# Kernel tuning notes

Hardware: AMD Instinct MI355X
Metric: run time of the kernel (lower is better)

The kernel has to match this reference:

```python
import jax, jax.numpy as jnp
import numpy as np

DEPTH = 10
LAMDA = 1e-3
EPS = 1e-7


def setup_inputs() -> dict:
    key = jax.random.key(0)
    k1, k2, k3, k4 = jax.random.split(key, 4)
    B, D, O = 16384, 512, 256
    N = 2 ** DEPTH - 1        # inner nodes
    L = 2 ** DEPTH            # leaves
    data = jax.random.normal(k1, (B, D), jnp.float32)
    # small scale on W keeps sigmoid away from saturation (like nn.Linear init)
    W = jax.random.normal(k2, (N, D + 1), jnp.float32) * 0.02
    beta = jax.random.normal(k3, (N,), jnp.float32)
    param = jax.random.normal(k4, (L, O), jnp.float32)
    return {"data": data, "W": W, "beta": beta, "param": param}


def reference(data, W, beta, param):
    B = data.shape[0]
    L = param.shape[0]
    # _data_augment_: prepend constant 1 as bias feature -> [B, D+1]
    x = jnp.concatenate([jnp.ones((B, 1), data.dtype), data], axis=1)
    # inner_nodes: sigmoid(beta * linear(x)) -> [B, N]
    p = jax.nn.sigmoid(beta * (x @ W.T))
    # per-node (go-left, go-right) probabilities -> [B, N, 2]
    path_prob = jnp.stack([p, 1.0 - p], axis=2)

    mu = jnp.ones((B, 1), data.dtype)          # path prob of root
    penalty = jnp.asarray(0.0, data.dtype)
    begin = 0
    for layer in range(DEPTH):                  # fixed small loop over depth
        n = 2 ** layer
        pp = path_prob[:, begin:begin + n, :].reshape(B, 2 * n)  # [B, 2n]
        mu_rep = jnp.repeat(mu, 2, axis=1)                        # [B, 2n]
        # vectorized form of the per-node penalty loop
        alpha = jnp.sum(pp * mu_rep, axis=0) / (jnp.sum(mu_rep, axis=0) + EPS)
        alpha = jnp.clip(alpha, EPS, 1.0 - EPS)
        coeff = LAMDA * (2.0 ** (-layer))
        penalty = penalty - coeff * 0.5 * jnp.sum(jnp.log(alpha) + jnp.log(1.0 - alpha))
        mu = mu_rep * pp
        begin += n

    # mu: [B, leaf_num]; leaf_nodes: mu @ softmax(param)
    dist = jax.nn.softmax(param, axis=1)       # [L, O]
    output = mu @ dist                          # [B, O]
    # greatest_path_probability: hard argmax leaf (one-hot @ dist == gather)
    ids = jnp.argmax(mu, axis=1)
    prediction = dist[ids]                      # [B, O]
    # LogProb=True
    return (jnp.log(prediction), jnp.log(output), penalty, W)
```

## Files before the change

### kernel.cpp

```cpp
#include <hip/hip_runtime.h>
#include <hip/hip_bf16.h>

#define B_ROWS 16384
#define DDIM   512
#define NNODES 1023
#define NLEAF  1024
#define ODIM   256
#define LAMDA  1e-3
#define EPSV   1e-7f

typedef __bf16 bf16x8v __attribute__((ext_vector_type(8)));
typedef _Float16 f16x8 __attribute__((ext_vector_type(8)));
typedef float  f32x16v __attribute__((ext_vector_type(16)));

__device__ __forceinline__ float bf2f(unsigned short u) {
    return __uint_as_float(((unsigned)u) << 16);
}

__device__ __forceinline__ void gload16h(const _Float16* g, _Float16* l) {
    __builtin_amdgcn_global_load_lds(
        (const __attribute__((address_space(1))) unsigned int*)g,
        (__attribute__((address_space(3))) unsigned int*)l, 16, 0, 0);
}
__device__ __forceinline__ void gload16b(const __hip_bfloat16* g, __hip_bfloat16* l) {
    __builtin_amdgcn_global_load_lds(
        (const __attribute__((address_space(1))) unsigned int*)g,
        (__attribute__((address_space(3))) unsigned int*)l, 16, 0, 0);
}

__global__ __launch_bounds__(256)
void prep_all(const float* __restrict__ data, const float* __restrict__ W,
              _Float16* __restrict__ Dh, _Float16* __restrict__ Dl,
              _Float16* __restrict__ Wh, _Float16* __restrict__ Wl,
              float* __restrict__ outW)
{
    if (blockIdx.x < 4096) {
        int idx = blockIdx.x * 256 + threadIdx.x;
        int b  = idx >> 6;
        int k8 = idx & 63;
        const float4 v0 = *reinterpret_cast<const float4*>(&data[(size_t)b * DDIM + k8 * 8]);
        const float4 v1 = *reinterpret_cast<const float4*>(&data[(size_t)b * DDIM + k8 * 8 + 4]);
        float a[8] = {v0.x, v0.y, v0.z, v0.w, v1.x, v1.y, v1.z, v1.w};
        __align__(16) _Float16 h[8], l[8];
#pragma unroll
        for (int j = 0; j < 8; ++j) {
            h[j] = (_Float16)a[j];
            l[j] = (_Float16)((a[j] - (float)h[j]) * 2048.f);
        }
        int by = b >> 8, tl = (b >> 5) & 7, ln = (b & 31) | ((k8 & 1) << 5), ks = k8 >> 1;
        size_t off = ((((size_t)by * 32 + ks) * 8 + tl) * 64 + ln) * 8;
        *reinterpret_cast<ulonglong2*>(&Dh[off]) = *reinterpret_cast<const ulonglong2*>(h);
        *reinterpret_cast<ulonglong2*>(&Dl[off]) = *reinterpret_cast<const ulonglong2*>(l);
    } else if (blockIdx.x < 4352) {
        int idx = (blockIdx.x - 4096) * 256 + threadIdx.x;
        int t  = idx & 255;
        int ks = (idx >> 8) & 31;
        int nb = idx >> 13;
        int tm = t >> 6, ln = t & 63;
        int node = nb * 128 + tm * 32 + (ln & 31);
        int k = ks * 16 + (ln >> 5) * 8;
        __align__(16) _Float16 h[8], l[8];
        if (node < NNODES) {
#pragma unroll
            for (int j = 0; j < 8; ++j) {
                float a = W[(size_t)node * 513 + 1 + k + j];
                h[j] = (_Float16)a;
                l[j] = (_Float16)((a - (float)h[j]) * 2048.f);
            }
        } else {
#pragma unroll
            for (int j = 0; j < 8; ++j) { h[j] = (_Float16)0.f; l[j] = (_Float16)0.f; }
        }
        size_t off = (size_t)idx * 8;
        *reinterpret_cast<ulonglong2*>(&Wh[off]) = *reinterpret_cast<const ulonglong2*>(h);
        *reinterpret_cast<ulonglong2*>(&Wl[off]) = *reinterpret_cast<const ulonglong2*>(l);
    } else {
        int i = (blockIdx.x - 4352) * 256 + threadIdx.x;
        if (i < NNODES * 513) outW[i] = W[i];
    }
}

__global__ __launch_bounds__(512, 2)
void gemm1_mfma(const _Float16* __restrict__ Wh, const _Float16* __restrict__ Wl,
                const _Float16* __restrict__ Dh, const _Float16* __restrict__ Dl,
                const float* __restrict__ W, const float* __restrict__ beta,
                float* __restrict__ PT)
{
    __shared__ _Float16 lds[2][24576];
    const int tid = threadIdx.x;
    const int lane = tid & 63;
    const int wv = tid >> 6;
    const int wm = wv & 1, wn = wv >> 1;
    const int id = blockIdx.x;
    const int xcd = id & 7, slot = id >> 3;
    const int bx = slot & 7;
    const int by = xcd * 8 + (slot >> 3);
    const size_t wofs = (size_t)bx * 65536 + tid * 8;
    const size_t dofs = (size_t)by * 131072 + tid * 8;

    f32x16v acc_h[2][2] = {};
    f32x16v acc_l[2][2] = {};

#define STAGE(buf, tt) do { \
        const size_t wo = wofs + (size_t)(tt) * 4096; \
        const size_t dd = dofs + (size_t)(tt) * 8192; \
        gload16h(Wh + wo,        &lds[buf][tid * 8]); \
        gload16h(Wl + wo,        &lds[buf][4096  + tid * 8]); \
        gload16h(Dh + dd,        &lds[buf][8192  + tid * 8]); \
        gload16h(Dh + dd + 4096, &lds[buf][12288 + tid * 8]); \
        gload16h(Dl + dd,        &lds[buf][16384 + tid * 8]); \
        gload16h(Dl + dd + 4096, &lds[buf][20480 + tid * 8]); \
    } while (0)

    STAGE(0, 0);
    asm volatile("s_waitcnt vmcnt(0)" ::: "memory");
    __builtin_amdgcn_s_barrier();

    for (int t = 0; t < 16; ++t) {
        const int cur = t & 1;
        if (t < 15) STAGE(cur ^ 1, t + 1);
        const _Float16* L = lds[cur];
#pragma unroll
        for (int kcl = 0; kcl < 2; ++kcl) {
            f16x8 ah[2], al[2], bh[2], bl[2];
#pragma unroll
            for (int i = 0; i < 2; ++i) {
                int ao = ((kcl * 4 + wm * 2 + i) * 64 + lane) * 8;
                ah[i] = *reinterpret_cast<const f16x8*>(&L[ao]);
                al[i] = *reinterpret_cast<const f16x8*>(&L[4096 + ao]);
            }
#pragma unroll
            for (int j = 0; j < 2; ++j) {
                int bo = ((kcl * 8 + wn * 2 + j) * 64 + lane) * 8;
                bh[j] = *reinterpret_cast<const f16x8*>(&L[8192 + bo]);
                bl[j] = *reinterpret_cast<const f16x8*>(&L[16384 + bo]);
            }
            __builtin_amdgcn_s_setprio(1);
#pragma unroll
            for (int i = 0; i < 2; ++i)
#pragma unroll
                for (int j = 0; j < 2; ++j) {
                    acc_h[i][j] = __builtin_amdgcn_mfma_f32_32x32x16_f16(ah[i], bh[j], acc_h[i][j], 0, 0, 0);
                    acc_l[i][j] = __builtin_amdgcn_mfma_f32_32x32x16_f16(ah[i], bl[j], acc_l[i][j], 0, 0, 0);
                    acc_l[i][j] = __builtin_amdgcn_mfma_f32_32x32x16_f16(al[i], bh[j], acc_l[i][j], 0, 0, 0);
                }
            __builtin_amdgcn_s_setprio(0);
        }
        if (t < 15) asm volatile("s_waitcnt vmcnt(0)" ::: "memory");
        __builtin_amdgcn_s_barrier();
    }
#undef STAGE

#pragma unroll
    for (int i = 0; i < 2; ++i) {
#pragma unroll
        for (int r = 0; r < 16; ++r) {
            int node = bx * 128 + wm * 64 + i * 32 + ((r & 3) + 8 * (r >> 2) + 4 * (lane >> 5));
            if (node < NNODES) {
                float w0 = W[(size_t)node * 513];
                float bt = beta[node];
#pragma unroll
                for (int j = 0; j < 2; ++j) {
                    float z = acc_h[i][j][r] + acc_l[i][j][r] * 4.8828125e-4f;
                    float s = bt * (z + w0);
                    float p = 1.f / (1.f + expf(-s));
                    PT[(size_t)node * B_ROWS + by * 256 + wn * 64 + j * 32 + (lane & 31)] = p;
                }
            }
        }
    }
}

__global__ __launch_bounds__(256, 4)
void tree_pass(const float* __restrict__ PT,
               __hip_bfloat16* __restrict__ MU2,
               float* __restrict__ pval,
               int*   __restrict__ pidx)
{
    const int tid = threadIdx.x;
    const int rb = blockIdx.x & 63;
    const int g  = blockIdx.x >> 6;
    const int b  = rb * 256 + tid;

    const int c4 = 15 + g;
    const int n3 = (c4 - 1) >> 1;
    const int n2 = (n3 - 1) >> 1;
    const int n1 = (n2 - 1) >> 1;
    const float pc4 = PT[(size_t)c4 * B_ROWS + b];
    const float pn3 = PT[(size_t)n3 * B_ROWS + b];
    const float pn2 = PT[(size_t)n2 * B_ROWS + b];
    const float pn1 = PT[(size_t)n1 * B_ROWS + b];
    const float pn0 = PT[b];
    float pre = ((c4 & 1) ? pn3 : 1.f - pn3)
              * ((n3 & 1) ? pn2 : 1.f - pn2)
              * ((n2 & 1) ? pn1 : 1.f - pn1)
              * ((n1 & 1) ? pn0 : 1.f - pn0);
    float root[2] = { pre * pc4, pre * (1.f - pc4) };

    __align__(16) __hip_bfloat16 mbv[64];
    float bestv = -1.f; int besti = 0;
#pragma unroll
    for (int ss = 0; ss < 2; ++ss) {
        const int t = 2 * g + ss;
        float s[32];
#pragma unroll
        for (int u = 1; u < 32; ++u) {
            int lvl = 31 - __clz(u);
            int node = ((32 << lvl) - 1) + t * (1 << lvl) + (u - (1 << lvl));
            s[u] = PT[(size_t)node * B_ROWS + b];
        }
        float w[64];
        w[1] = root[ss];
#pragma unroll
        for (int u = 1; u < 32; ++u) {
            w[2 * u]     = w[u] * s[u];
            w[2 * u + 1] = w[u] * (1.f - s[u]);
        }
#pragma unroll
        for (int q = 0; q < 32; ++q) {
            float lv = w[32 + q];
            mbv[ss * 32 + q] = __float2bfloat16(lv);
            if (lv > bestv) { bestv = lv; besti = t * 32 + q; }
        }
    }
    {
        const int mb_ = b >> 7, mt_ = (b >> 5) & 3, lnlo = b & 31;
        const ulonglong2* src = reinterpret_cast<const ulonglong2*>(mbv);
#pragma unroll
        for (int c = 0; c < 4; ++c) {
            size_t base16 = (((size_t)mb_ * 64 + g * 4 + c) * 4 + mt_) * 64;
            *reinterpret_cast<ulonglong2*>(&MU2[(base16 + lnlo) * 8])      = src[c * 2];
            *reinterpret_cast<ulonglong2*>(&MU2[(base16 + 32 + lnlo) * 8]) = src[c * 2 + 1];
        }
    }
    pval[(size_t)g * B_ROWS + b] = bestv;
    pidx[(size_t)g * B_ROWS + b] = besti;
}

__global__ __launch_bounds__(256)
void colsum(const __hip_bfloat16* __restrict__ MU2, float* __restrict__ partial)
{
    __shared__ float red[4][2][8];
    const int blk = blockIdx.x;
    const int kc = blk >> 2, mbg = blk & 3;
    const int t = threadIdx.x;
    const int w = t >> 6, ln = t & 63;
    float a[8] = {0.f, 0.f, 0.f, 0.f, 0.f, 0.f, 0.f, 0.f};
    for (int it = 0; it < 32; ++it) {
        int it2 = it * 4 + w;
        int mb = mbg * 32 + (it2 >> 2), mt = it2 & 3;
        size_t a16 = (((size_t)mb * 64 + kc) * 4 + mt) * 64 + ln;
        ulonglong2 u = *reinterpret_cast<const ulonglong2*>(&MU2[a16 * 8]);
        const unsigned short* hs = reinterpret_cast<const unsigned short*>(&u);
#pragma unroll
        for (int j = 0; j < 8; ++j) a[j] += bf2f(hs[j]);
    }
#pragma unroll
    for (int m = 1; m < 32; m <<= 1)
#pragma unroll
        for (int j = 0; j < 8; ++j) a[j] += __shfl_xor(a[j], m, 64);
    if ((ln & 31) == 0) {
#pragma unroll
        for (int j = 0; j < 8; ++j) red[w][ln >> 5][j] = a[j];
    }
    __syncthreads();
    if (t < 16) {
        float s = red[0][t >> 3][t & 7] + red[1][t >> 3][t & 7]
                + red[2][t >> 3][t & 7] + red[3][t >> 3][t & 7];
        partial[(size_t)mbg * NLEAF + kc * 16 + t] = s;
    }
}

__global__ __launch_bounds__(256)
void softmax_param(const float* __restrict__ param,
                   float* __restrict__ logdist,
                   __hip_bfloat16* __restrict__ DT2)
{
    __shared__ float red[4], red2[4];
    int l = blockIdx.x;
    int o = threadIdx.x;
    float x = param[(size_t)l * ODIM + o];
    float m = x;
#pragma unroll
    for (int s = 1; s < 64; s <<= 1) m = fmaxf(m, __shfl_xor(m, s, 64));
    if ((o & 63) == 0) red[o >> 6] = m;
    __syncthreads();
    m = fmaxf(fmaxf(red[0], red[1]), fmaxf(red[2], red[3]));
    float e = expf(x - m);
    float s = e;
#pragma unroll
    for (int k = 1; k < 64; k <<= 1) s += __shfl_xor(s, k, 64);
    if ((o & 63) == 0) red2[o >> 6] = s;
    __syncthreads();
    s = red2[0] + red2[1] + red2[2] + red2[3];
    float d = e / s;
    logdist[(size_t)l * ODIM + o] = logf(d);
    int kc = l >> 4, kk = l & 15;
    int lane = (o & 31) | ((kk >> 3) << 5);
    DT2[(((size_t)kc * 8 + (o >> 5)) * 64 + lane) * 8 + (kk & 7)] = __float2bfloat16(d);
}

__global__ __launch_bounds__(256)
void penalty_kernel(const float* __restrict__ partial, float* __restrict__ out_pen)
{
    __shared__ float M[2048];
    __shared__ double dred[256];
    int tid = threadIdx.x;
    for (int i = tid; i < 1024; i += 256)
        M[1024 + i] = partial[i] + partial[NLEAF + i] + partial[2 * NLEAF + i] + partial[3 * NLEAF + i];
    __syncthreads();
    for (int n = 512; n >= 1; n >>= 1) {
        for (int u = n + tid; u < 2 * n; u += 256) M[u] = M[2 * u] + M[2 * u + 1];
        __syncthreads();
    }
    double acc = 0.0;
    for (int u = 2 + tid; u < 2048; u += 256) {
        int lvl = 31 - __clz(u);
        float a = M[u] / (M[u >> 1] + EPSV);
        a = fminf(fmaxf(a, EPSV), 1.f - EPSV);
        float term = logf(a) + logf(1.f - a);
        acc -= ldexp((double)LAMDA * 0.5, 1 - lvl) * (double)term;
    }
    dred[tid] = acc;
    __syncthreads();
    for (int s = 128; s > 0; s >>= 1) {
        if (tid < s) dred[tid] += dred[tid + s];
        __syncthreads();
    }
    if (tid == 0) out_pen[0] = (float)dred[0];
}

__global__ __launch_bounds__(256)
void gemm2_log(const __hip_bfloat16* __restrict__ MU2,
               const __hip_bfloat16* __restrict__ DT2,
               float* __restrict__ out1)
{
    __shared__ __hip_bfloat16 ldsA[2][2048];
    __shared__ __hip_bfloat16 ldsB[2][8192];
    const int tid = threadIdx.x;
    const int lane = tid & 63;
    const int w = tid >> 6;
    const int blk = blockIdx.x;
    const int m0 = blk * 64;
    const int mb = blk >> 1;
    const int mtbase = (blk & 1) * 2;
    const int s_kcl = tid >> 7, s_mti = (tid >> 6) & 1, s_ln = tid & 63;

    f32x16v acc[2][2] = {};

#define STAGE2(buf, kc0) do { \
        size_t sa16 = (((size_t)mb * 64 + (kc0) + s_kcl) * 4 + mtbase + s_mti) * 64 + s_ln; \
        gload16b(MU2 + sa16 * 8, &ldsA[buf][tid * 8]); \
        gload16b(DT2 + ((size_t)(kc0) * 512 + tid) * 8,             &ldsB[buf][tid * 8]); \
        gload16b(DT2 + ((size_t)(kc0) * 512 + 256 + tid) * 8,       &ldsB[buf][2048 + tid * 8]); \
        gload16b(DT2 + ((size_t)((kc0) + 1) * 512 + tid) * 8,       &ldsB[buf][4096 + tid * 8]); \
        gload16b(DT2 + ((size_t)((kc0) + 1) * 512 + 256 + tid) * 8, &ldsB[buf][6144 + tid * 8]); \
    } while (0)

    STAGE2(0, 0);
    for (int it = 0; it < 32; ++it) {
        const int cur = it & 1;
        if (it + 1 < 32) {
            STAGE2(cur ^ 1, 2 * (it + 1));
            asm volatile("s_waitcnt vmcnt(5)" ::: "memory");
        } else {
            asm volatile("s_waitcnt vmcnt(0)" ::: "memory");
        }
        __builtin_amdgcn_s_barrier();
        bf16x8v a[2][2], bb[2][2];
#pragma unroll
        for (int kcl = 0; kcl < 2; ++kcl)
#pragma unroll
            for (int i = 0; i < 2; ++i) {
                a[kcl][i]  = *reinterpret_cast<const bf16x8v*>(&ldsA[cur][((kcl * 2 + i) * 64 + lane) * 8]);
                bb[kcl][i] = *reinterpret_cast<const bf16x8v*>(&ldsB[cur][((kcl * 8 + 2 * w + i) * 64 + lane) * 8]);
            }
        __builtin_amdgcn_s_setprio(1);
#pragma unroll
        for (int kcl = 0; kcl < 2; ++kcl)
#pragma unroll
            for (int i = 0; i < 2; ++i)
#pragma unroll
                for (int j = 0; j < 2; ++j)
                    acc[i][j] = __builtin_amdgcn_mfma_f32_32x32x16_bf16(a[kcl][i], bb[kcl][j], acc[i][j], 0, 0, 0);
        __builtin_amdgcn_s_setprio(0);
        asm volatile("s_waitcnt lgkmcnt(0)" ::: "memory");
        __builtin_amdgcn_s_barrier();
    }
#undef STAGE2
#pragma unroll
    for (int i = 0; i < 2; ++i)
#pragma unroll
        for (int j = 0; j < 2; ++j)
#pragma unroll
            for (int r = 0; r < 16; ++r) {
                int row = m0 + i * 32 + (r & 3) + 8 * (r >> 2) + 4 * (lane >> 5);
                int col = w * 64 + j * 32 + (lane & 31);
                out1[(size_t)row * ODIM + col] = logf(acc[i][j][r]);
            }
}

__global__ __launch_bounds__(256)
void argmax_gather(const float* __restrict__ pval, const int* __restrict__ pidx,
                   const float* __restrict__ logdist, float* __restrict__ out0)
{
    __shared__ int sid[64];
    const int blk = blockIdx.x;
    const int t = threadIdx.x;
    if (t < 64) {
        int row = blk * 64 + t;
        float bv = -1.f; int bi = 0;
        for (int g = 0; g < 16; ++g) {
            float v = pval[(size_t)g * B_ROWS + row];
            if (v > bv) { bv = v; bi = pidx[(size_t)g * B_ROWS + row]; }
        }
        sid[t] = bi;
    }
    __syncthreads();
    for (int rr = 0; rr < 64; ++rr) {
        int id = sid[rr];
        out0[(size_t)(blk * 64 + rr) * ODIM + t] = logdist[(size_t)id * ODIM + t];
    }
}

extern "C" void kernel_launch(void* const* d_in, const int* in_sizes, int n_in,
                              void* d_out, int out_size, void* d_ws, size_t ws_size,
                              hipStream_t stream)
{
    (void)in_sizes; (void)n_in; (void)out_size; (void)ws_size;
    const float* data  = (const float*)d_in[0];
    const float* W     = (const float*)d_in[1];
    const float* beta  = (const float*)d_in[2];
    const float* param = (const float*)d_in[3];
    float* out = (float*)d_out;

    char* ws = (char*)d_ws;
    size_t off = 0;
    float* PT = (float*)(ws + off);                   off += (size_t)NNODES * B_ROWS * 4;
    char* X = ws + off;                               off += 2 * 1048576 + 2 * 16777216;
    _Float16* Wh = (_Float16*)(X);
    _Float16* Wl = (_Float16*)(X + 1048576);
    _Float16* Dh = (_Float16*)(X + 2 * 1048576);
    _Float16* Dl = (_Float16*)(X + 2 * 1048576 + 16777216);
    __hip_bfloat16* MU2 = (__hip_bfloat16*)(X + 2 * 1048576);
    __hip_bfloat16* DT2 = (__hip_bfloat16*)(ws + off); off += (size_t)ODIM * NLEAF * 2;
    float* logdist = (float*)(ws + off);              off += (size_t)NLEAF * ODIM * 4;
    float* partial = (float*)(ws + off);              off += (size_t)4 * NLEAF * 4;
    float* pval    = (float*)(ws + off);              off += (size_t)16 * B_ROWS * 4;
    int*   pidx    = (int*)(ws + off);                off += (size_t)16 * B_ROWS * 4;

    float* out_logpred = out;
    float* out_logout  = out + (size_t)B_ROWS * ODIM;
    float* out_pen     = out + 2 * (size_t)B_ROWS * ODIM;
    float* out_W       = out_pen + 1;

    prep_all<<<6404, 256, 0, stream>>>(data, W, Dh, Dl, Wh, Wl, out_W);
    softmax_param<<<NLEAF, 256, 0, stream>>>(param, logdist, DT2);

    gemm1_mfma<<<512, 512, 0, stream>>>(Wh, Wl, Dh, Dl, W, beta, PT);

    tree_pass<<<1024, 256, 0, stream>>>(PT, MU2, pval, pidx);
    colsum<<<256, 256, 0, stream>>>(MU2, partial);
    penalty_kernel<<<1, 256, 0, stream>>>(partial, out_pen);

    gemm2_log<<<B_ROWS / 64, 256, 0, stream>>>(MU2, DT2, out_logout);
    argmax_gather<<<B_ROWS / 64, 256, 0, stream>>>(pval, pidx, logdist, out_logpred);
}
```

Before: 162.0 us.

## Triple-buffer GEMM1 pipeline and merge small kernels to cut launches

The first GEMM moves from double to triple-buffered LDS staging with a prefetch distance of two tiles, using partial vmcnt waits. It also splits each tile's compute into two fragment-load/MFMA phases separated by barriers. Separately, softmax_param is folded into prep_all, argmax_gather into colsum, and penalty into gemm2, going from 8 launches to 5 to cut launch and tail overhead. The trade-offs are more LDS per block, which may lower occupancy at 2 blocks/CU, and extra barriers inside the GEMM loop.

```diff
diff --git a/kernel.cpp b/kernel.cpp
--- a/kernel.cpp
+++ b/kernel.cpp
@@ -30,10 +30,13 @@
 
 __global__ __launch_bounds__(256)
 void prep_all(const float* __restrict__ data, const float* __restrict__ W,
+              const float* __restrict__ param,
               _Float16* __restrict__ Dh, _Float16* __restrict__ Dl,
               _Float16* __restrict__ Wh, _Float16* __restrict__ Wl,
-              float* __restrict__ outW)
-{
+              float* __restrict__ outW,
+              float* __restrict__ logdist, __hip_bfloat16* __restrict__ DT2)
+{
+    __shared__ float red[4], red2[4];
     if (blockIdx.x < 4096) {
         int idx = blockIdx.x * 256 + threadIdx.x;
         int b  = idx >> 6;
@@ -74,9 +77,31 @@
         size_t off = (size_t)idx * 8;
         *reinterpret_cast<ulonglong2*>(&Wh[off]) = *reinterpret_cast<const ulonglong2*>(h);
         *reinterpret_cast<ulonglong2*>(&Wl[off]) = *reinterpret_cast<const ulonglong2*>(l);
-    } else {
+    } else if (blockIdx.x < 6404) {
         int i = (blockIdx.x - 4352) * 256 + threadIdx.x;
         if (i < NNODES * 513) outW[i] = W[i];
+    } else {
+        int l = blockIdx.x - 6404;
+        int o = threadIdx.x;
+        float x = param[(size_t)l * ODIM + o];
+        float m = x;
+#pragma unroll
+        for (int s = 1; s < 64; s <<= 1) m = fmaxf(m, __shfl_xor(m, s, 64));
+        if ((o & 63) == 0) red[o >> 6] = m;
+        __syncthreads();
+        m = fmaxf(fmaxf(red[0], red[1]), fmaxf(red[2], red[3]));
+        float e = expf(x - m);
+        float s = e;
+#pragma unroll
+        for (int k = 1; k < 64; k <<= 1) s += __shfl_xor(s, k, 64);
+        if ((o & 63) == 0) red2[o >> 6] = s;
+        __syncthreads();
+        s = red2[0] + red2[1] + red2[2] + red2[3];
+        float d = e / s;
+        logdist[(size_t)l * ODIM + o] = logf(d);
+        int kc = l >> 4, kk = l & 15;
+        int lane = (o & 31) | ((kk >> 3) << 5);
+        DT2[(((size_t)kc * 8 + (o >> 5)) * 64 + lane) * 8 + (kk & 7)] = __float2bfloat16(d);
     }
 }
 
@@ -86,7 +111,7 @@
                 const float* __restrict__ W, const float* __restrict__ beta,
                 float* __restrict__ PT)
 {
-    __shared__ _Float16 lds[2][24576];
+    __shared__ _Float16 lds[3][24576];
     const int tid = threadIdx.x;
     const int lane = tid & 63;
     const int wv = tid >> 6;
@@ -112,44 +137,63 @@
         gload16h(Dl + dd + 4096, &lds[buf][20480 + tid * 8]); \
     } while (0)
 
+#define LOADFRAG(L, kcl) do { \
+        _Pragma("unroll") \
+        for (int i = 0; i < 2; ++i) { \
+            int ao = (((kcl) * 4 + wm * 2 + i) * 64 + lane) * 8; \
+            ah[i] = *reinterpret_cast<const f16x8*>(&(L)[ao]); \
+            al[i] = *reinterpret_cast<const f16x8*>(&(L)[4096 + ao]); \
+        } \
+        _Pragma("unroll") \
+        for (int j = 0; j < 2; ++j) { \
+            int bo = (((kcl) * 8 + wn * 2 + j) * 64 + lane) * 8; \
+            bh[j] = *reinterpret_cast<const f16x8*>(&(L)[8192 + bo]); \
+            bl[j] = *reinterpret_cast<const f16x8*>(&(L)[16384 + bo]); \
+        } \
+    } while (0)
+
+#define MFMA12() do { \
+        _Pragma("unroll") \
+        for (int i = 0; i < 2; ++i) \
+        _Pragma("unroll") \
+        for (int j = 0; j < 2; ++j) { \
+            acc_h[i][j] = __builtin_amdgcn_mfma_f32_32x32x16_f16(ah[i], bh[j], acc_h[i][j], 0, 0, 0); \
+            acc_l[i][j] = __builtin_amdgcn_mfma_f32_32x32x16_f16(ah[i], bl[j], acc_l[i][j], 0, 0, 0); \
+            acc_l[i][j] = __builtin_amdgcn_mfma_f32_32x32x16_f16(al[i], bh[j], acc_l[i][j], 0, 0, 0); \
+        } \
+    } while (0)
+
     STAGE(0, 0);
-    asm volatile("s_waitcnt vmcnt(0)" ::: "memory");
+    STAGE(1, 1);
+    asm volatile("s_waitcnt vmcnt(6)" ::: "memory");
     __builtin_amdgcn_s_barrier();
 
     for (int t = 0; t < 16; ++t) {
-        const int cur = t & 1;
-        if (t < 15) STAGE(cur ^ 1, t + 1);
-        const _Float16* L = lds[cur];
-#pragma unroll
-        for (int kcl = 0; kcl < 2; ++kcl) {
-            f16x8 ah[2], al[2], bh[2], bl[2];
-#pragma unroll
-            for (int i = 0; i < 2; ++i) {
-                int ao = ((kcl * 4 + wm * 2 + i) * 64 + lane) * 8;
-                ah[i] = *reinterpret_cast<const f16x8*>(&L[ao]);
-                al[i] = *reinterpret_cast<const f16x8*>(&L[4096 + ao]);
-            }
-#pragma unroll
-            for (int j = 0; j < 2; ++j) {
-                int bo = ((kcl * 8 + wn * 2 + j) * 64 + lane) * 8;
-                bh[j] = *reinterpret_cast<const f16x8*>(&L[8192 + bo]);
-                bl[j] = *reinterpret_cast<const f16x8*>(&L[16384 + bo]);
-            }
-            __builtin_amdgcn_s_setprio(1);
-#pragma unroll
-            for (int i = 0; i < 2; ++i)
-#pragma unroll
-                for (int j = 0; j < 2; ++j) {
-                    acc_h[i][j] = __builtin_amdgcn_mfma_f32_32x32x16_f16(ah[i], bh[j], acc_h[i][j], 0, 0, 0);
-                    acc_l[i][j] = __builtin_amdgcn_mfma_f32_32x32x16_f16(ah[i], bl[j], acc_l[i][j], 0, 0, 0);
-                    acc_l[i][j] = __builtin_amdgcn_mfma_f32_32x32x16_f16(al[i], bh[j], acc_l[i][j], 0, 0, 0);
-                }
-            __builtin_amdgcn_s_setprio(0);
-        }
-        if (t < 15) asm volatile("s_waitcnt vmcnt(0)" ::: "memory");
+        const _Float16* L = lds[t % 3];
+        f16x8 ah[2], al[2], bh[2], bl[2];
+
+        LOADFRAG(L, 0);
+        if (t + 2 < 16) STAGE((t + 2) % 3, t + 2);
+        __builtin_amdgcn_s_barrier();
+        asm volatile("s_waitcnt lgkmcnt(0)" ::: "memory");
+        __builtin_amdgcn_s_setprio(1);
+        MFMA12();
+        __builtin_amdgcn_s_setprio(0);
+        __builtin_amdgcn_s_barrier();
+
+        LOADFRAG(L, 1);
+        __builtin_amdgcn_s_barrier();
+        asm volatile("s_waitcnt lgkmcnt(0)" ::: "memory");
+        __builtin_amdgcn_s_setprio(1);
+        MFMA12();
+        __builtin_amdgcn_s_setprio(0);
+        if (t < 14) asm volatile("s_waitcnt vmcnt(6)" ::: "memory");
+        else        asm volatile("s_waitcnt vmcnt(0)" ::: "memory");
         __builtin_amdgcn_s_barrier();
     }
 #undef STAGE
+#undef LOADFRAG
+#undef MFMA12
 
 #pragma unroll
     for (int i = 0; i < 2; ++i) {
@@ -238,106 +282,96 @@
 }
 
 __global__ __launch_bounds__(256)
-void colsum(const __hip_bfloat16* __restrict__ MU2, float* __restrict__ partial)
+void colsum_argmax(const __hip_bfloat16* __restrict__ MU2, float* __restrict__ partial,
+                   const float* __restrict__ pval, const int* __restrict__ pidx,
+                   const float* __restrict__ logdist, float* __restrict__ out0)
 {
     __shared__ float red[4][2][8];
-    const int blk = blockIdx.x;
-    const int kc = blk >> 2, mbg = blk & 3;
+    __shared__ int sid[64];
     const int t = threadIdx.x;
-    const int w = t >> 6, ln = t & 63;
-    float a[8] = {0.f, 0.f, 0.f, 0.f, 0.f, 0.f, 0.f, 0.f};
-    for (int it = 0; it < 32; ++it) {
-        int it2 = it * 4 + w;
-        int mb = mbg * 32 + (it2 >> 2), mt = it2 & 3;
-        size_t a16 = (((size_t)mb * 64 + kc) * 4 + mt) * 64 + ln;
-        ulonglong2 u = *reinterpret_cast<const ulonglong2*>(&MU2[a16 * 8]);
-        const unsigned short* hs = reinterpret_cast<const unsigned short*>(&u);
-#pragma unroll
-        for (int j = 0; j < 8; ++j) a[j] += bf2f(hs[j]);
-    }
-#pragma unroll
-    for (int m = 1; m < 32; m <<= 1)
-#pragma unroll
-        for (int j = 0; j < 8; ++j) a[j] += __shfl_xor(a[j], m, 64);
-    if ((ln & 31) == 0) {
-#pragma unroll
-        for (int j = 0; j < 8; ++j) red[w][ln >> 5][j] = a[j];
-    }
-    __syncthreads();
-    if (t < 16) {
-        float s = red[0][t >> 3][t & 7] + red[1][t >> 3][t & 7]
-                + red[2][t >> 3][t & 7] + red[3][t >> 3][t & 7];
-        partial[(size_t)mbg * NLEAF + kc * 16 + t] = s;
+    if (blockIdx.x < 256) {
+        const int blk = blockIdx.x;
+        const int kc = blk >> 2, mbg = blk & 3;
+        const int w = t >> 6, ln = t & 63;
+        float a[8] = {0.f, 0.f, 0.f, 0.f, 0.f, 0.f, 0.f, 0.f};
+        for (int it = 0; it < 32; ++it) {
+            int it2 = it * 4 + w;
+            int mb = mbg * 32 + (it2 >> 2), mt = it2 & 3;
+            size_t a16 = (((size_t)mb * 64 + kc) * 4 + mt) * 64 + ln;
+            ulonglong2 u = *reinterpret_cast<const ulonglong2*>(&MU2[a16 * 8]);
+            const unsigned short* hs = reinterpret_cast<const unsigned short*>(&u);
+#pragma unroll
+            for (int j = 0; j < 8; ++j) a[j] += bf2f(hs[j]);
+        }
+#pragma unroll
+        for (int m = 1; m < 32; m <<= 1)
+#pragma unroll
+            for (int j = 0; j < 8; ++j) a[j] += __shfl_xor(a[j], m, 64);
+        if ((ln & 31) == 0) {
+#pragma unroll
+            for (int j = 0; j < 8; ++j) red[w][ln >> 5][j] = a[j];
+        }
+        __syncthreads();
+        if (t < 16) {
+            float s = red[0][t >> 3][t & 7] + red[1][t >> 3][t & 7]
+                    + red[2][t >> 3][t & 7] + red[3][t >> 3][t & 7];
+            partial[(size_t)mbg * NLEAF + kc * 16 + t] = s;
+        }
+    } else {
+        const int blk = blockIdx.x - 256;
+        if (t < 64) {
+            int row = blk * 64 + t;
+            float bv = -1.f; int bi = 0;
+            for (int g = 0; g < 16; ++g) {
+                float v = pval[(size_t)g * B_ROWS + row];
+                if (v > bv) { bv = v; bi = pidx[(size_t)g * B_ROWS + row]; }
+            }
+            sid[t] = bi;
+        }
+        __syncthreads();
+        for (int rr = 0; rr < 64; ++rr) {
+            int id = sid[rr];
+            out0[(size_t)(blk * 64 + rr) * ODIM + t] = logdist[(size_t)id * ODIM + t];
+        }
     }
 }
 
 __global__ __launch_bounds__(256)
-void softmax_param(const float* __restrict__ param,
-                   float* __restrict__ logdist,
-                   __hip_bfloat16* __restrict__ DT2)
-{
-    __shared__ float red[4], red2[4];
-    int l = blockIdx.x;
-    int o = threadIdx.x;
-    float x = param[(size_t)l * ODIM + o];
-    float m = x;
-#pragma unroll
-    for (int s = 1; s < 64; s <<= 1) m = fmaxf(m, __shfl_xor(m, s, 64));
-    if ((o & 63) == 0) red[o >> 6] = m;
-    __syncthreads();
-    m = fmaxf(fmaxf(red[0], red[1]), fmaxf(red[2], red[3]));
-    float e = expf(x - m);
-    float s = e;
-#pragma unroll
-    for (int k = 1; k < 64; k <<= 1) s += __shfl_xor(s, k, 64);
-    if ((o & 63) == 0) red2[o >> 6] = s;
-    __syncthreads();
-    s = red2[0] + red2[1] + red2[2] + red2[3];
-    float d = e / s;
-    logdist[(size_t)l * ODIM + o] = logf(d);
-    int kc = l >> 4, kk = l & 15;
-    int lane = (o & 31) | ((kk >> 3) << 5);
-    DT2[(((size_t)kc * 8 + (o >> 5)) * 64 + lane) * 8 + (kk & 7)] = __float2bfloat16(d);
-}
-
-__global__ __launch_bounds__(256)
-void penalty_kernel(const float* __restrict__ partial, float* __restrict__ out_pen)
-{
+void gemm2_penalty(const __hip_bfloat16* __restrict__ MU2,
+                   const __hip_bfloat16* __restrict__ DT2,
+                   float* __restrict__ out1,
+                   const float* __restrict__ partial, float* __restrict__ out_pen)
+{
+    __shared__ __hip_bfloat16 ldsA[2][2048];
+    __shared__ __hip_bfloat16 ldsB[2][8192];
     __shared__ float M[2048];
     __shared__ double dred[256];
-    int tid = threadIdx.x;
-    for (int i = tid; i < 1024; i += 256)
-        M[1024 + i] = partial[i] + partial[NLEAF + i] + partial[2 * NLEAF + i] + partial[3 * NLEAF + i];
-    __syncthreads();
-    for (int n = 512; n >= 1; n >>= 1) {
-        for (int u = n + tid; u < 2 * n; u += 256) M[u] = M[2 * u] + M[2 * u + 1];
-        __syncthreads();
-    }
-    double acc = 0.0;
-    for (int u = 2 + tid; u < 2048; u += 256) {
-        int lvl = 31 - __clz(u);
-        float a = M[u] / (M[u >> 1] + EPSV);
-        a = fminf(fmaxf(a, EPSV), 1.f - EPSV);
-        float term = logf(a) + logf(1.f - a);
-        acc -= ldexp((double)LAMDA * 0.5, 1 - lvl) * (double)term;
-    }
-    dred[tid] = acc;
-    __syncthreads();
-    for (int s = 128; s > 0; s >>= 1) {
-        if (tid < s) dred[tid] += dred[tid + s];
-        __syncthreads();
-    }
-    if (tid == 0) out_pen[0] = (float)dred[0];
-}
-
-__global__ __launch_bounds__(256)
-void gemm2_log(const __hip_bfloat16* __restrict__ MU2,
-               const __hip_bfloat16* __restrict__ DT2,
-               float* __restrict__ out1)
-{
-    __shared__ __hip_bfloat16 ldsA[2][2048];
-    __shared__ __hip_bfloat16 ldsB[2][8192];
     const int tid = threadIdx.x;
+    if (blockIdx.x == 256) {
+        for (int i = tid; i < 1024; i += 256)
+            M[1024 + i] = partial[i] + partial[NLEAF + i] + partial[2 * NLEAF + i] + partial[3 * NLEAF + i];
+        __syncthreads();
+        for (int n = 512; n >= 1; n >>= 1) {
+            for (int u = n + tid; u < 2 * n; u += 256) M[u] = M[2 * u] + M[2 * u + 1];
+            __syncthreads();
+        }
+        double acc = 0.0;
+        for (int u = 2 + tid; u < 2048; u += 256) {
+            int lvl = 31 - __clz(u);
+            float a = M[u] / (M[u >> 1] + EPSV);
+            a = fminf(fmaxf(a, EPSV), 1.f - EPSV);
+            float term = logf(a) + logf(1.f - a);
+            acc -= ldexp((double)LAMDA * 0.5, 1 - lvl) * (double)term;
+        }
+        dred[tid] = acc;
+        __syncthreads();
+        for (int s = 128; s > 0; s >>= 1) {
+            if (tid < s) dred[tid] += dred[tid + s];
+            __syncthreads();
+        }
+        if (tid == 0) out_pen[0] = (float)dred[0];
+        return;
+    }
     const int lane = tid & 63;
     const int w = tid >> 6;
     const int blk = blockIdx.x;
@@ -398,29 +432,6 @@
                 int col = w * 64 + j * 32 + (lane & 31);
                 out1[(size_t)row * ODIM + col] = logf(acc[i][j][r]);
             }
-}
-
-__global__ __launch_bounds__(256)
-void argmax_gather(const float* __restrict__ pval, const int* __restrict__ pidx,
-                   const float* __restrict__ logdist, float* __restrict__ out0)
-{
-    __shared__ int sid[64];
-    const int blk = blockIdx.x;
-    const int t = threadIdx.x;
-    if (t < 64) {
-        int row = blk * 64 + t;
-        float bv = -1.f; int bi = 0;
-        for (int g = 0; g < 16; ++g) {
-            float v = pval[(size_t)g * B_ROWS + row];
-            if (v > bv) { bv = v; bi = pidx[(size_t)g * B_ROWS + row]; }
-        }
-        sid[t] = bi;
-    }
-    __syncthreads();
-    for (int rr = 0; rr < 64; ++rr) {
-        int id = sid[rr];
-        out0[(size_t)(blk * 64 + rr) * ODIM + t] = logdist[(size_t)id * ODIM + t];
-    }
 }
 
 extern "C" void kernel_launch(void* const* d_in, const int* in_sizes, int n_in,
@@ -454,15 +465,13 @@
     float* out_pen     = out + 2 * (size_t)B_ROWS * ODIM;
     float* out_W       = out_pen + 1;
 
-    prep_all<<<6404, 256, 0, stream>>>(data, W, Dh, Dl, Wh, Wl, out_W);
-    softmax_param<<<NLEAF, 256, 0, stream>>>(param, logdist, DT2);
+    prep_all<<<7428, 256, 0, stream>>>(data, W, param, Dh, Dl, Wh, Wl, out_W, logdist, DT2);
 
     gemm1_mfma<<<512, 512, 0, stream>>>(Wh, Wl, Dh, Dl, W, beta, PT);
 
     tree_pass<<<1024, 256, 0, stream>>>(PT, MU2, pval, pidx);
-    colsum<<<256, 256, 0, stream>>>(MU2, partial);
-    penalty_kernel<<<1, 256, 0, stream>>>(partial, out_pen);
-
-    gemm2_log<<<B_ROWS / 64, 256, 0, stream>>>(MU2, DT2, out_logout);
-    argmax_gather<<<B_ROWS / 64, 256, 0, stream>>>(pval, pidx, logdist, out_logpred);
-}
+
+    colsum_argmax<<<512, 256, 0, stream>>>(MU2, partial, pval, pidx, logdist, out_logpred);
+
+    gemm2_penalty<<<257, 256, 0, stream>>>(MU2, DT2, out_logout, partial, out_pen);
+}
```

Result: faster. 151.3 us (-6.6%).
